# Performance work log

Hardware: AMD Instinct MI355X
Metric: run time of the kernel (lower is better)

Reference implementation:

```python
import math
import jax, jax.numpy as jnp
import numpy as np

SAMPLE_RATIO = 0.25
K_NN = 5


def grid_index(loc_orig, H, W):
    # loc in [-1,1] -> nearest grid cell index (row-major)
    loc = jnp.clip(loc_orig, -1.0, 1.0) * 0.5 + 0.5
    ix = jnp.clip(jnp.round(loc[..., 0] * (W - 1)).astype(jnp.int32), 0, W - 1)
    iy = jnp.clip(jnp.round(loc[..., 1] * (H - 1)).astype(jnp.int32), 0, H - 1)
    return iy * W + ix  # [B, N0]


def token2map(x, loc_orig, idx_agg, H, W):
    # scatter token features (replicated to original points) into HxW grid, cell-average
    B, N, C = x.shape
    N0 = idx_agg.shape[1]
    idx_hw = grid_index(loc_orig, H, W)
    off = jnp.arange(B, dtype=jnp.int32)[:, None]
    idx_hw_flat = (idx_hw + off * (H * W)).reshape(-1)
    value = jnp.ones((B * N0,), x.dtype)
    all_w = jax.ops.segment_sum(value, idx_hw_flat, num_segments=B * H * W) + 1e-6
    value = value / all_w[idx_hw_flat]
    x_src = jnp.take_along_axis(x, idx_agg[..., None], axis=1).reshape(B * N0, C)
    x_map = jax.ops.segment_sum(x_src * value[:, None], idx_hw_flat, num_segments=B * H * W)
    return x_map.reshape(B, H, W, C).transpose(0, 3, 1, 2)  # [B,C,H,W]


def map2token(x_map, N, loc_orig, idx_agg, agg_weight):
    # gather grid features back to tokens, weighted by per-token-normalized agg_weight
    B, C, H, W = x_map.shape
    N0 = idx_agg.shape[1]
    idx_hw = grid_index(loc_orig, H, W)
    off = jnp.arange(B, dtype=jnp.int32)[:, None]
    idx_tok_flat = (idx_agg + off * N).reshape(-1)
    idx_hw_flat = (idx_hw + off * (H * W)).reshape(-1)
    value = agg_weight.reshape(-1).astype(x_map.dtype)
    all_w = jax.ops.segment_sum(value, idx_tok_flat, num_segments=B * N) + 1e-6
    value = value / all_w[idx_tok_flat]
    feat = x_map.transpose(0, 2, 3, 1).reshape(B * H * W, C)[idx_hw_flat]
    out = jax.ops.segment_sum(feat * value[:, None], idx_tok_flat, num_segments=B * N)
    return out.reshape(B, N, C)


def cluster_dpc_knn(x, Ns, k):
    # DPC-KNN clustering (no_grad in original -> stop_gradient)
    B, N, C = x.shape
    x = jax.lax.stop_gradient(x)
    x2 = jnp.sum(x * x, axis=-1)
    d2 = x2[:, :, None] + x2[:, None, :] - 2.0 * jnp.einsum('bic,bjc->bij', x, x)
    dist = jnp.sqrt(jnp.maximum(d2, 0.0)) / jnp.sqrt(jnp.asarray(C, x.dtype))
    dist_nearest = -jax.lax.top_k(-dist, k)[0]                 # k smallest dists (incl self)
    density = jnp.exp(-jnp.mean(dist_nearest ** 2, axis=-1))    # [B,N]
    # deterministic tiny tie-break noise (original uses torch.rand*1e-6)
    density = density + jax.random.uniform(jax.random.key(42), density.shape, density.dtype) * 1e-6
    mask = (density[:, None, :] > density[:, :, None]).astype(x.dtype)
    dist_max = jnp.max(dist.reshape(B, -1), axis=-1)[:, None, None]
    dist_ind = jnp.min(dist * mask + dist_max * (1.0 - mask), axis=-1)
    score = dist_ind * density
    index_down = jax.lax.top_k(score, Ns)[1]                    # [B,Ns] cluster centers
    dist_c = jnp.take_along_axis(dist, index_down[:, :, None], axis=1)  # [B,Ns,N]
    idx_cluster = jnp.argmin(dist_c, axis=1).astype(jnp.int32)  # [B,N]
    # centers belong to their own cluster
    flat = (index_down + jnp.arange(B)[:, None] * N).reshape(-1)
    own = jnp.tile(jnp.arange(Ns, dtype=jnp.int32), B)
    idx_cluster = idx_cluster.reshape(-1).at[flat].set(own).reshape(B, N)
    return idx_cluster


def merge_tokens(x, idx_cluster, Ns, weight, idx_agg):
    # weighted average of tokens per cluster; propagate mapping/weights to original points
    B, N, C = x.shape
    idx = (idx_cluster + jnp.arange(B, dtype=jnp.int32)[:, None] * Ns).reshape(-1)
    w = weight.reshape(-1)
    all_w = jax.ops.segment_sum(w, idx, num_segments=B * Ns) + 1e-6
    nw = w / all_w[idx]
    x_merged = jax.ops.segment_sum(x.reshape(B * N, C) * nw[:, None], idx,
                                   num_segments=B * Ns).reshape(B, Ns, C)
    norm_weight = nw.reshape(B, N, 1)
    idx_agg_new = jnp.take_along_axis(idx_cluster, idx_agg, axis=1)          # [B,N0]
    weight_t = jnp.take_along_axis(norm_weight, idx_agg[..., None], axis=1)  # [B,N0,1]
    return x_merged, idx_agg_new, weight_t


def ctm_forward(x, loc_orig, idx_agg, agg_weight, conv_w, conv_b, skip_w, ln_g, ln_b,
                conf_w, conf_b, H, W):
    B, N, C = x.shape
    x_map = token2map(x, loc_orig, idx_agg, H, W)
    x_map = jax.lax.conv_general_dilated(
        x_map, conv_w, window_strides=(2, 2), padding=((1, 1), (1, 1)),
        dimension_numbers=('NCHW', 'OIHW', 'NCHW')) + conv_b[None, :, None, None]
    xt = map2token(x_map, N, loc_orig, idx_agg, agg_weight) + x @ skip_w.T
    mu = jnp.mean(xt, axis=-1, keepdims=True)
    var = jnp.mean((xt - mu) ** 2, axis=-1, keepdims=True)
    xt = (xt - mu) / jnp.sqrt(var + 1e-5) * ln_g + ln_b
    conf = xt @ conf_w.T + conf_b          # [B,N,1]
    weight = jnp.exp(conf)
    Ns = max(math.ceil(N * SAMPLE_RATIO), 1)
    idx_cluster = cluster_dpc_knn(xt, Ns, K_NN)
    x_down, idx_agg_down, weight_t = merge_tokens(xt, idx_cluster, Ns, weight, idx_agg)
    agg_weight_down = agg_weight * weight_t
    agg_weight_down = agg_weight_down / jnp.max(agg_weight_down, axis=1, keepdims=True)
    # down_block is identity in this reference
    return x_down, idx_agg_down, agg_weight_down


def setup_inputs() -> dict:
    key = jax.random.key(0)
    ks = jax.random.split(key, 10)
    B, N, C, C2, H, W = 4, 3136, 64, 128, 56, 56
    return {
        'x': jax.random.normal(ks[0], (B, N, C), jnp.float32),
        'loc_orig': jax.random.normal(ks[1], (B, N, 2), jnp.float32),
        'idx_agg': jax.random.randint(ks[2], (B, N), 0, N),
        'agg_weight': jax.random.uniform(ks[3], (B, N, 1), jnp.float32, 0.1, 1.0),
        'conv_w': jax.random.normal(ks[4], (C2, C, 3, 3), jnp.float32) * 0.02,
        'conv_b': jnp.zeros((C2,), jnp.float32),
        'skip_w': jax.random.normal(ks[5], (C2, C), jnp.float32) * 0.02,
        'ln_g': jnp.ones((C2,), jnp.float32),
        'ln_b': jnp.zeros((C2,), jnp.float32),
        'conf_w': jax.random.normal(ks[6], (1, C2), jnp.float32) * 0.02,
        'conf_b': jnp.zeros((1,), jnp.float32),
        'H': 56,
        'W': 56,
    }


def reference(x, loc_orig, idx_agg, agg_weight, conv_w, conv_b, skip_w, ln_g, ln_b,
              conf_w, conf_b, H, W):
    return ctm_forward(x, loc_orig, idx_agg, agg_weight, conv_w, conv_b, skip_w,
                       ln_g, ln_b, conf_w, conf_b, H, W)
```

## Files before the change

kernel.cpp:

```cpp
#include <hip/hip_runtime.h>
#include <math.h>
#include <float.h>

#define Bq   4
#define Nq   3136
#define Cq   64
#define C2q  128
#define Hq   56
#define Wq   56
#define HWq  (Hq*Wq)
#define HOq  28
#define WOq  28
#define HWOq (HOq*WOq)
#define NSq  784
#define KNN  5
#define BNq  (Bq*Nq)

#define T64   64
#define KC    32
#define NIT64 (Nq/T64)
#define NPAIR (NIT64*(NIT64+1)/2)
#define NSPL  8
#define NSPA  2
#define LDP   34

__device__ __constant__ int c_spl[NSPL + 1]  = {0, 7, 13, 19, 25, 31, 37, 43, 49};
__device__ __constant__ int c_spla[NSPA + 1] = {0, 7, 13};

typedef unsigned int   u32;
typedef unsigned long long u64;
typedef __attribute__((ext_vector_type(4))) double d64x4;

static __device__ __forceinline__ void atomicMaxPosD(double* p, double v) {
    atomicMax((u64*)p, (u64)__double_as_longlong(v));
}
static __device__ __forceinline__ int clampTok(int t) {
    return min(max(t, 0), Nq - 1);
}

static __device__ __forceinline__ u64 encD(double d) {
    u64 u = (u64)__double_as_longlong(d);
    return (u >> 63) ? ~u : (u | 0x8000000000000000ULL);
}
static __device__ __forceinline__ double decD(u64 u) {
    u64 o = (u >> 63) ? (u ^ 0x8000000000000000ULL) : ~u;
    return __longlong_as_double((long long)o);
}
#define ENC_DBL_MAX 0xFFEFFFFFFFFFFFFFULL

static __device__ __forceinline__ void ins5(double* a, double v) {
    if (v < a[KNN - 1]) {
        a[KNN - 1] = v;
        #pragma unroll
        for (int m = KNN - 1; m > 0; m--)
            if (a[m] < a[m - 1]) { double t = a[m]; a[m] = a[m - 1]; a[m - 1] = t; }
    }
}
static __device__ __forceinline__ void cex(double& a, double& b) {
    double lo = fmin(a, b), hi = fmax(a, b); a = lo; b = hi;
}
static __device__ __forceinline__ void merge5(double* a, const double* p) {
    double t0 = fmin(a[0], p[4]);
    double t1 = fmin(a[1], p[3]);
    double t2 = fmin(a[2], p[2]);
    double t3 = fmin(a[3], p[1]);
    double t4 = fmin(a[4], p[0]);
    cex(t0, t1); cex(t1, t2); cex(t2, t3); cex(t3, t4);
    cex(t0, t1); cex(t1, t2); cex(t2, t3);
    cex(t0, t1); cex(t1, t2);
    cex(t0, t1);
    a[0] = t0; a[1] = t1; a[2] = t2; a[3] = t3; a[4] = t4;
}

static __device__ __forceinline__ int mfma_mode_probe(int l4, int l15) {
    d64x4 p;
    #pragma unroll
    for (int v = 0; v < 4; v++) p[v] = 0.0;
    double a1 = (l4 == 0) ? (double)(16 * l15) : 0.0;
    double b1 = (l4 == 0) ? 1.0 : 0.0;
    p = __builtin_amdgcn_mfma_f64_16x16x4f64(a1, b1, p, 0, 0, 0);
    double a2 = (l4 == 0) ? 1.0 : 0.0;
    double b2 = (l4 == 0) ? (double)l15 : 0.0;
    p = __builtin_amdgcn_mfma_f64_16x16x4f64(a2, b2, p, 0, 0, 0);
    bool ok0 = true, ok1 = true;
    #pragma unroll
    for (int v = 0; v < 4; v++) {
        ok0 = ok0 && (p[v] == (double)(16 * (4 * l4 + v) + l15));
        ok1 = ok1 && (p[v] == (double)(16 * (l4 + 4 * v) + l15));
    }
    return __all(ok0) ? 0 : (__all(ok1) ? 1 : 2);
}

static __device__ __forceinline__ u32 rotl32(u32 x, int d) { return (x << d) | (x >> (32 - d)); }
static __device__ __forceinline__ float tf_uniform(int t) {
    const u32 k0 = 0u, k1 = 42u;
    const u32 ks2 = k0 ^ k1 ^ 0x1BD11BDAu;
    u32 ks[3] = { k0, k1, ks2 };
    bool lo = (t < 6272);
    u32 cx0 = lo ? (u32)t : (u32)(t - 6272);
    u32 cx1 = lo ? (u32)(t + 6272) : (u32)t;
    u32 x0 = cx0 + ks[0];
    u32 x1 = cx1 + ks[1];
    const int R0[4] = {13, 15, 26, 6};
    const int R1[4] = {17, 29, 16, 24};
// ... 125 lines not shown
    #pragma unroll 16
    for (int k = 0; k < Cq; k++) acc += (double)xr[k] * (double)sw[k];
    __shared__ double slot[4][2];
    double s = acc;
    #pragma unroll
    for (int m = 1; m <= 32; m <<= 1) s += __shfl_xor(s, m);
    if (lane == 0) slot[0][w] = s;
    __syncthreads();
    double mu = (slot[0][0] + slot[0][1]) * (1.0 / C2q);
    double d = acc - mu;
    s = d * d;
    #pragma unroll
    for (int m = 1; m <= 32; m <<= 1) s += __shfl_xor(s, m);
    if (lane == 0) slot[1][w] = s;
    __syncthreads();
    double var = (slot[1][0] + slot[1][1]) * (1.0 / C2q);
    double v = d / sqrt(var + 1e-5) * (double)lng[c] + (double)lnb[c];
    row[c] = v;
    s = v * v;
    #pragma unroll
    for (int m = 1; m <= 32; m <<= 1) s += __shfl_xor(s, m);
    if (lane == 0) slot[2][w] = s;
    double s2 = v * (double)confw[c];
    #pragma unroll
    for (int m = 1; m <= 32; m <<= 1) s2 += __shfl_xor(s2, m);
    if (lane == 0) slot[3][w] = s2;
    __syncthreads();
    if (c == 0) {
        x2o[bn] = slot[2][0] + slot[2][1];
        weightv[bn] = exp(slot[3][0] + slot[3][1] + (double)confb[0]);
    }
}


__global__ __launch_bounds__(256, 2)
void ctm_pass1(const double* __restrict__ xt, const double* __restrict__ x2,
               double* pbest, double* pmax) {
    __shared__ double sBB[2][T64][LDP];
    __shared__ double sx2j[2][T64];
    int blk = blockIdx.x;
    int b  = blk & (Bq - 1);
    int s  = (blk >> 2) & (NSPL - 1);
    int it = blk >> 5;
    int tid = threadIdx.x;
    const double* xtb = xt + (size_t)b * Nq * C2q;
    const double* x2b = x2 + (size_t)b * Nq;
    int i0 = it * T64;
    int jt_beg = c_spl[s], jt_end = c_spl[s + 1];

    int wv = tid >> 6, ln = tid & 63;
    int l15 = ln & 15, l4 = ln >> 4;
    int mode = mfma_mode_probe(l4, l15);

    if (mode < 2) {
        int rw[4];
        #pragma unroll
        for (int v = 0; v < 4; v++) rw[v] = (mode == 0) ? (4 * l4 + v) : (l4 + 4 * v);
        int rbase = i0 + wv * 16;
        double a_reg[4][8];
        const double* arow = xtb + (size_t)(i0 + wv * 16 + l15) * C2q + l4;
        #pragma unroll
        for (int kc = 0; kc < 4; kc++)
            #pragma unroll
            for (int st = 0; st < 8; st++)
                a_reg[kc][st] = arow[kc * KC + 4 * st];
        double x2i[4];
        #pragma unroll
        for (int v = 0; v < 4; v++) x2i[v] = x2b[rbase + rw[v]];
        double best[4][KNN]; double mx[4];
        #pragma unroll
        for (int v = 0; v < 4; v++) {
            mx[v] = -DBL_MAX;
            #pragma unroll
            for (int k = 0; k < KNN; k++) best[v][k] = DBL_MAX;
        }
        {
            int j0 = jt_beg * T64;
            #pragma unroll
            for (int w = 0; w < 4; w++) {
                int idx = tid + w * 256; int r = idx >> 4, c = (idx & 15) * 2;
                *(double2*)&sBB[0][r][c] = *(const double2*)&xtb[(size_t)(j0 + r) * C2q + c];
            }
            if (tid < T64) sx2j[0][tid] = x2b[j0 + tid];
        }
        __syncthreads();
        int q = 0;
        for (int jt = jt_beg; jt < jt_end; jt++) {
            int j0 = jt * T64;
            d64x4 acc[4];
            #pragma unroll
            for (int bc = 0; bc < 4; bc++)
                #pragma unroll
                for (int v = 0; v < 4; v++) acc[bc][v] = 0.0;
            #pragma unroll
            for (int kc = 0; kc < 4; kc++) {
                const int cb = kc & 1, nb = cb ^ 1, nkc = (kc + 1) & 3;
                const bool lastk = (kc == 3);
                bool hn = !lastk || (jt + 1 < jt_end);
                int nj0 = lastk ? j0 + T64 : j0;
                double2 sreg[4]; double xr = 0.0;
                if (hn) {
                    #pragma unroll
                    for (int w = 0; w < 4; w++) {
                        int idx = tid + w * 256; int r = idx >> 4, c = (idx & 15) * 2;
                        sreg[w] = *(const double2*)&xtb[(size_t)(nj0 + r) * C2q + nkc * KC + c];
                    }
                    if (lastk && tid < T64) xr = x2b[nj0 + tid];
                }
                #pragma unroll
                for (int st = 0; st < 8; st++) {
                    double av = a_reg[kc][st];
                    #pragma unroll
                    for (int bc = 0; bc < 4; bc++) {
                        double bv = sBB[cb][bc * 16 + l15][4 * st + l4];
                        acc[bc] = __builtin_amdgcn_mfma_f64_16x16x4f64(av, bv, acc[bc], 0, 0, 0);
                    }
                }
                if (hn) {
                    #pragma unroll
                    for (int w = 0; w < 4; w++) {
                        int idx = tid + w * 256; int r = idx >> 4, c = (idx & 15) * 2;
                        *(double2*)&sBB[nb][r][c] = sreg[w];
                    }
                    if (lastk && tid < T64) sx2j[q ^ 1][tid] = xr;
                }
                __syncthreads();
            }
            #pragma unroll
            for (int bc = 0; bc < 4; bc++) {
                double xj = sx2j[q][bc * 16 + l15];
                #pragma unroll
                for (int v = 0; v < 4; v++) {
                    double d2 = x2i[v] + xj - 2.0 * acc[bc][v];
                    mx[v] = fmax(mx[v], d2);
                    ins5(best[v], d2);
                }
            }
            q ^= 1;
        }
        for (int m = 1; m <= 8; m <<= 1) {
            #pragma unroll
            for (int v = 0; v < 4; v++) {
                double p[KNN];
                #pragma unroll
                for (int k = 0; k < KNN; k++) p[k] = __shfl_xor(best[v][k], m);
                mx[v] = fmax(mx[v], __shfl_xor(mx[v], m));
                merge5(best[v], p);
            }
        }
        if (l15 == 0) {
            #pragma unroll
            for (int v = 0; v < 4; v++) {
                int gi = b * Nq + rbase + rw[v];
                size_t base = ((size_t)s * BNq + gi) * KNN;
                #pragma unroll
                for (int k = 0; k < KNN; k++) pbest[base + k] = best[v][k];
                pmax[(size_t)s * BNq + gi] = mx[v];
            }
        }
    } else {
        double (*sA)[LDP] = sBB[0];
        double (*sB)[LDP] = sBB[1];
        int tx = tid & 15, ty = tid >> 4;
        double x2i[4];
        #pragma unroll
        for (int r = 0; r < 4; r++) x2i[r] = x2b[i0 + ty + 16 * r];
        double best[4][KNN]; double mx[4];
        #pragma unroll
        for (int r = 0; r < 4; r++) {
            mx[r] = -DBL_MAX;
            #pragma unroll
            for (int k = 0; k < KNN; k++) best[r][k] = DBL_MAX;
        }
        for (int jt = jt_beg; jt < jt_end; jt++) {
            int j0 = jt * T64;
            double acc[4][4];
            #pragma unroll
            for (int r = 0; r < 4; r++)
                #pragma unroll
                for (int q = 0; q < 4; q++) acc[r][q] = 0.0;
            for (int kc = 0; kc < 4; kc++) {
                __syncthreads();
                #pragma unroll
                for (int idx = tid; idx < T64 * KC / 2; idx += 256) {
                    int r = idx >> 4, c = (idx & 15) * 2;
                    *(double2*)&sA[r][c] = *(const double2*)&xtb[(size_t)(i0 + r) * C2q + kc * KC + c];
                    *(double2*)&sB[r][c] = *(const double2*)&xtb[(size_t)(j0 + r) * C2q + kc * KC + c];
                }
                if (kc == 0 && tid < T64) sx2j[0][tid] = x2b[j0 + tid];
                __syncthreads();
                #pragma unroll 4
                for (int cc = 0; cc < KC; cc += 2) {
                    double2 xi[4], xj[4];
                    #pragma unroll
                    for (int r = 0; r < 4; r++) xi[r] = *(const double2*)&sA[ty + 16 * r][cc];
                    #pragma unroll
                    for (int q = 0; q < 4; q++) xj[q] = *(const double2*)&sB[tx + 16 * q][cc];
                    #pragma unroll
                    for (int r = 0; r < 4; r++)
                        #pragma unroll
                        for (int q = 0; q < 4; q++) acc[r][q] += xi[r].x * xj[q].x;
                    #pragma unroll
                    for (int r = 0; r < 4; r++)
                        #pragma unroll
                        for (int q = 0; q < 4; q++) acc[r][q] += xi[r].y * xj[q].y;
                }
            }
            #pragma unroll
            for (int r = 0; r < 4; r++)
                #pragma unroll
                for (int q = 0; q < 4; q++) {
                    double d2 = x2i[r] + sx2j[0][tx + 16 * q] - 2.0 * acc[r][q];
                    mx[r] = fmax(mx[r], d2);
                    ins5(best[r], d2);
                }
        }
        for (int m = 1; m <= 8; m <<= 1) {
            #pragma unroll
            for (int r = 0; r < 4; r++) {
                double p[KNN];
                #pragma unroll
                for (int k = 0; k < KNN; k++) p[k] = __shfl_xor(best[r][k], m);
                mx[r] = fmax(mx[r], __shfl_xor(mx[r], m));
                merge5(best[r], p);
            }
        }
        if (tx == 0) {
            #pragma unroll
            for (int r = 0; r < 4; r++) {
                int gi = b * Nq + i0 + ty + 16 * r;
                size_t base = ((size_t)s * BNq + gi) * KNN;
                #pragma unroll
                for (int k = 0; k < KNN; k++) pbest[base + k] = best[r][k];
                pmax[(size_t)s * BNq + gi] = mx[r];
            }
        }
    }
}

__global__ void ctm_merge1(const double* __restrict__ pbest, const double* __restrict__ pmax,
                           double* density, double* maxd2) {
    int t = blockIdx.x * blockDim.x + threadIdx.x;
    if (t >= BNq) return;
    double a[KNN];
    #pragma unroll
    for (int k = 0; k < KNN; k++) a[k] = pbest[(size_t)t * KNN + k];
    double mxv = pmax[t];
    #pragma unroll
    for (int s = 1; s < NSPL; s++) {
        double p[KNN];
        #pragma unroll
        for (int k = 0; k < KNN; k++) p[k] = pbest[((size_t)s * BNq + t) * KNN + k];
        merge5(a, p);
        mxv = fmax(mxv, pmax[(size_t)s * BNq + t]);
    }
    double sum = 0.0;
    #pragma unroll
    for (int k = 0; k < KNN; k++) sum += fmax(a[k], 0.0);
    density[t] = exp(-sum / (double)(C2q * KNN)) + (double)(tf_uniform(t) * 1e-6f);
    atomicMaxPosD(&maxd2[t / Nq], mxv);
}

__global__ __launch_bounds__(1024)
void ctm_sortd(const double* __restrict__ density, int* perm) {
    __shared__ double s[4096];
    __shared__ int   si[4096];
    int b = blockIdx.x, tid = threadIdx.x;
    for (int i = tid; i < 4096; i += 1024) {
        if (i < Nq) {
            double v = density[b * Nq + i];
            s[i] = isnan(v) ? -DBL_MAX : v;
            si[i] = i;
        } else { s[i] = -DBL_MAX; si[i] = 0x7fffffff; }
    }
    __syncthreads();
    for (int k = 2; k <= 4096; k <<= 1) {
        for (int j = k >> 1; j > 0; j >>= 1) {
            for (int i = tid; i < 4096; i += 1024) {
                int ixj = i ^ j;
                if (ixj > i) {
                    double s1 = s[i], s2 = s[ixj];
                    int i1 = si[i], i2 = si[ixj];
                    bool before_ij = (s1 > s2) || (s1 == s2 && i1 < i2);
                    bool before_ji = (s2 > s1) || (s2 == s1 && i2 < i1);
                    bool doswap = ((i & k) == 0) ? before_ji : before_ij;
                    if (doswap) { s[i] = s2; s[ixj] = s1; si[i] = i2; si[ixj] = i1; }
                }
            }
            __syncthreads();
        }
    }
    for (int t = tid; t < Nq; t += 1024) {
        int v = si[t];
        perm[b * Nq + t] = ((unsigned)v < (unsigned)Nq) ? v : 0;
    }
}

__global__ void ctm_initmin(u64* pmin2u) {
    int t = blockIdx.x * blockDim.x + threadIdx.x;
    if (t < BNq) pmin2u[t] = ENC_DBL_MAX;
}

__global__ __launch_bounds__(256, 2)
void ctm_pass2t(const double* __restrict__ xt, const double* __restrict__ x2,
                const double* __restrict__ density, const int* __restrict__ perm,
                u64* pmin2u) {
    __shared__ double sBB[2][T64][LDP];
    __shared__ double sx2j[T64];
    __shared__ double sdj[T64];
    __shared__ int    sI[T64];
    __shared__ int    sJ[T64];
    __shared__ double sp[4][T64];
    int blk = blockIdx.x;
    int b = blk & (Bq - 1);
    int p = blk >> 2;
    int it = (int)((sqrt(8.0 * (double)p + 1.0) - 1.0) * 0.5);
    while ((it + 1) * (it + 2) / 2 <= p) ++it;
    while (it * (it + 1) / 2 > p) --it;
    int jt = p - it * (it + 1) / 2;
    int i0 = it * T64, j0 = jt * T64;
    int tid = threadIdx.x;
    const double* xtb = xt + (size_t)b * Nq * C2q;
    const double* x2b = x2 + (size_t)b * Nq;
    const double* db  = density + (size_t)b * Nq;
    const int* pb = perm + b * Nq;
    if (tid < T64) sI[tid] = pb[i0 + tid];
    else if (tid < 2 * T64) sJ[tid - T64] = pb[j0 + tid - T64];
    __syncthreads();
    int wv = tid >> 6, ln = tid & 63;
    int l15 = ln & 15, l4 = ln >> 4;
    int mode = mfma_mode_probe(l4, l15);

    if (mode < 2) {
        int rw[4];
        #pragma unroll
        for (int v = 0; v < 4; v++) rw[v] = (mode == 0) ? (4 * l4 + v) : (l4 + 4 * v);
        int rloc = wv * 16;
        double a_reg[4][8];
        const double* arow = xtb + (size_t)sI[rloc + l15] * C2q + l4;
        #pragma unroll
        for (int kc = 0; kc < 4; kc++)
            #pragma unroll
            for (int st = 0; st < 8; st++)
                a_reg[kc][st] = arow[kc * KC + 4 * st];
        double x2i[4], di[4];
        #pragma unroll
        for (int v = 0; v < 4; v++) {
            int o = sI[rloc + rw[v]];
            x2i[v] = x2b[o];
            di[v]  = db[o];
        }
        #pragma unroll
        for (int w = 0; w < 4; w++) {
            int idx = tid + w * 256; int r = idx >> 4, c = (idx & 15) * 2;
            *(double2*)&sBB[0][r][c] = *(const double2*)&xtb[(size_t)sJ[r] * C2q + c];
        }
        if (tid < T64) { int o = sJ[tid]; sx2j[tid] = x2b[o]; sdj[tid] = db[o]; }
        __syncthreads();
        d64x4 acc[4];
        #pragma unroll
        for (int bc = 0; bc < 4; bc++)
            #pragma unroll
            for (int v = 0; v < 4; v++) acc[bc][v] = 0.0;
        #pragma unroll
        for (int kc = 0; kc < 4; kc++) {
            const int cb = kc & 1, nb = cb ^ 1;
            const bool hn = (kc < 3);
            double2 sreg[4];
            if (hn) {
                #pragma unroll
                for (int w = 0; w < 4; w++) {
                    int idx = tid + w * 256; int r = idx >> 4, c = (idx & 15) * 2;
                    sreg[w] = *(const double2*)&xtb[(size_t)sJ[r] * C2q + (kc + 1) * KC + c];
                }
            }
            #pragma unroll
            for (int st = 0; st < 8; st++) {
                double av = a_reg[kc][st];
                #pragma unroll
                for (int bc = 0; bc < 4; bc++) {
                    double bv = sBB[cb][bc * 16 + l15][4 * st + l4];
                    acc[bc] = __builtin_amdgcn_mfma_f64_16x16x4f64(av, bv, acc[bc], 0, 0, 0);
                }
            }
            if (hn) {
                #pragma unroll
                for (int w = 0; w < 4; w++) {
                    int idx = tid + w * 256; int r = idx >> 4, c = (idx & 15) * 2;
                    *(double2*)&sBB[nb][r][c] = sreg[w];
                }
            }
            __syncthreads();
        }
        double mn[4];
        #pragma unroll
        for (int v = 0; v < 4; v++) mn[v] = DBL_MAX;
        #pragma unroll
        for (int bc = 0; bc < 4; bc++) {
            double xj = sx2j[bc * 16 + l15];
            double dj = sdj[bc * 16 + l15];
            #pragma unroll
            for (int v = 0; v < 4; v++) {
                double d2 = x2i[v] + xj - 2.0 * acc[bc][v];
                if (dj > di[v]) mn[v] = fmin(mn[v], d2);
            }
        }
        for (int m = 1; m <= 8; m <<= 1) {
            #pragma unroll
            for (int v = 0; v < 4; v++) mn[v] = fmin(mn[v], __shfl_xor(mn[v], m));
        }
        if (l15 == 0) {
            #pragma unroll
            for (int v = 0; v < 4; v++)
                if (mn[v] < DBL_MAX)
                    atomicMin(&pmin2u[b * Nq + i0 + rloc + rw[v]], encD(mn[v]));
        }
    } else {
        int rl = tid & 63;
        int cg = tid >> 6;
        int ro = sI[rl];
        double x2i = x2b[ro];
        double di = db[ro];
        const double* xr = xtb + (size_t)ro * C2q;
        double mn = DBL_MAX;
        for (int cc = 0; cc < 16; cc++) {
            int co = sJ[cg * 16 + cc];
            if (db[co] > di) {
                const double* xc = xtb + (size_t)co * C2q;
                double dot = 0.0;
                for (int k = 0; k < C2q; k++) dot += xr[k] * xc[k];
                mn = fmin(mn, x2i + x2b[co] - 2.0 * dot);
            }
        }
        sp[cg][rl] = mn;
        __syncthreads();
        if (cg == 0) {
            mn = fmin(fmin(sp[0][rl], sp[1][rl]), fmin(sp[2][rl], sp[3][rl]));
            if (mn < DBL_MAX)
                atomicMin(&pmin2u[b * Nq + i0 + rl], encD(mn));
        }
    }
}

__global__ void ctm_merge2t(const u64* __restrict__ pmin2u, const double* __restrict__ maxd2,
                            const double* __restrict__ density, const int* __restrict__ perm,
                            double* score) {
    int t = blockIdx.x * blockDim.x + threadIdx.x;
    if (t >= BNq) return;
    int b = t / Nq;
    double m = decD(pmin2u[t]);
    double mm = fmin(maxd2[b], m);
    int orig = b * Nq + perm[t];
    score[orig] = sqrt(fmax(mm, 0.0)) / sqrt((double)C2q) * density[orig];
}

__global__ __launch_bounds__(1024)
void ctm_sort(const double* __restrict__ score, int* index_down) {
    __shared__ double s[4096];
    __shared__ int   si[4096];
    int b = blockIdx.x, tid = threadIdx.x;
    for (int i = tid; i < 4096; i += 1024) {
        if (i < Nq) {
            double v = score[b * Nq + i];
            s[i] = isnan(v) ? -DBL_MAX : v;
// ... 168 lines not shown
            }
            #pragma unroll
            for (int r = 0; r < 4; r++)
                #pragma unroll
                for (int q = 0; q < 4; q++) {
                    int sc = j0 + tx + 16 * q;
                    double d = fmax(x2i[r] + sx2c[tx + 16 * q] - 2.0 * acc[r][q], 0.0);
                    if (sc < NSq && (d < bd[r] || (d == bd[r] && sc < bs[r]))) { bd[r] = d; bs[r] = sc; }
                }
        }
        for (int m = 1; m <= 8; m <<= 1) {
            #pragma unroll
            for (int r = 0; r < 4; r++) {
                double pd = __shfl_xor(bd[r], m);
                int    ps = __shfl_xor(bs[r], m);
                if (pd < bd[r] || (pd == bd[r] && ps < bs[r])) { bd[r] = pd; bs[r] = ps; }
            }
        }
        if (tx == 0) {
            #pragma unroll
            for (int r = 0; r < 4; r++) {
                int gi = b * Nq + i0 + ty + 16 * r;
                pbd[(size_t)s * BNq + gi] = bd[r];
                pbs[(size_t)s * BNq + gi] = bs[r];
            }
        }
    }
}

__global__ void ctm_merge3(const double* __restrict__ pbd, const int* __restrict__ pbs,
                           int* idx_cluster) {
    int t = blockIdx.x * blockDim.x + threadIdx.x;
    if (t >= BNq) return;
    double d0 = pbd[t];          int s0 = pbs[t];
    double d1 = pbd[BNq + t];    int s1 = pbs[BNq + t];
    bool take1 = (d1 < d0) || (d1 == d0 && s1 < s0);
    idx_cluster[t] = take1 ? s1 : s0;
}

__global__ void ctm_override(const int* __restrict__ index_down, int* idx_cluster) {
    int t = blockIdx.x * blockDim.x + threadIdx.x;
    if (t >= Bq * NSq) return;
    int b = t / NSq, sc = t - b * NSq;
    int j = index_down[t];
    if ((unsigned)j < (unsigned)Nq) idx_cluster[b * Nq + j] = sc;
}

__global__ void ctm_zeromerged(double* xmerged) {
    int t = blockIdx.x * blockDim.x + threadIdx.x;
    if (t < Bq * NSq * C2q) xmerged[t] = 0.0;
}

__global__ void ctm_merge_w(const int* __restrict__ idx_cluster, const double* __restrict__ weightv,
                            double* allwc) {
    int t = blockIdx.x * blockDim.x + threadIdx.x;
    if (t >= BNq) return;
    int b = t / Nq;
    int sc = min(max(idx_cluster[t], 0), NSq - 1);
    atomicAdd(&allwc[b * NSq + sc], weightv[t]);
}

__global__ void ctm_merge_x(const int* __restrict__ idx_cluster, const double* __restrict__ weightv,
                            const double* __restrict__ allwc, const double* __restrict__ xt,
                            double* nw, double* xmerged) {
    int id = blockIdx.x * blockDim.x + threadIdx.x;
    if (id >= BNq * C2q) return;
    int t = id / C2q, c = id - t * C2q;
    int b = t / Nq;
    int sc = min(max(idx_cluster[t], 0), NSq - 1);
    double nv = weightv[t] / (allwc[b * NSq + sc] + 1e-6);
// ... 45 lines not shown
    (void)in_sizes; (void)n_in;

    char* w = (char*)d_ws;
    size_t off = 0;
    auto alloc = [&](size_t bytes) -> void* {
        void* p = w + off; off = (off + bytes + 255) & ~(size_t)255; return p;
    };

    int*    cnt56   = (int*)   alloc((size_t)BNq * 4);
    double* allwtok = (double*)alloc((size_t)BNq * 8);
    double* xt      = (double*)alloc((size_t)BNq * C2q * 8);
    double* arena   = (double*)alloc((size_t)Bq * HWq * Cq * 8);
    double* allwc   = (double*)alloc((size_t)Bq * NSq * 8);
    double* maxawd  = (double*)alloc((size_t)Bq * 8);
    double* maxd2   = (double*)alloc((size_t)Bq * 8);
    size_t zero_bytes = off;
    int*    cell56   = (int*)   alloc((size_t)BNq * 4);
    int*    cell28   = (int*)   alloc((size_t)BNq * 4);
    double* xmap28T  = (double*)alloc((size_t)Bq * HWOq * C2q * 8);
    float*  wT       = (float*) alloc((size_t)C2q * Cq * 9 * 4);
    double* x2       = (double*)alloc((size_t)BNq * 8);
    double* density  = (double*)alloc((size_t)BNq * 8);
    double* score    = (double*)alloc((size_t)BNq * 8);
    int*    indexdn  = (int*)   alloc((size_t)Bq * NSq * 4);
    int*    idxclu   = (int*)   alloc((size_t)BNq * 4);
    double* nw       = (double*)alloc((size_t)BNq * 8);
    double* weightv  = (double*)alloc((size_t)BNq * 8);
    double* awd      = (double*)alloc((size_t)BNq * 8);
    double* pbest    = (double*)alloc((size_t)NSPL * BNq * KNN * 8);
    double* pmax     = (double*)alloc((size_t)NSPL * BNq * 8);
    double* pbd      = (double*)alloc((size_t)NSPA * BNq * 8);
    int*    pbs      = (int*)   alloc((size_t)NSPA * BNq * 4);
    size_t required = off;

    int* perm   = (int*)pbest;
    u64* pmin2u = (u64*)((char*)pbest + 131072);

    const int tb = 256;
    float* out = (float*)d_out;

    if (ws_size < required) {
        ctm_fallback<<<(out_size + tb - 1) / tb, tb, 0, stream>>>(out, out_size);
        return;
    }

    double* xmap56T = arena;
    double* xmerged = arena;

    hipMemsetAsync(d_ws, 0, zero_bytes, stream);

    ctm_prep<<<(BNq + tb - 1) / tb, tb, 0, stream>>>(loc, idxag, aggw, cell56, cell28, cnt56, allwtok);
    ctm_wt<<<((C2q * Cq * 9) + tb - 1) / tb, tb, 0, stream>>>(convw, wT);
    ctm_t2m<<<((BNq * Cq) + tb - 1) / tb, tb, 0, stream>>>(x, idxag, cell56, cnt56, xmap56T);
    ctm_conv<<<Bq * (HWOq / 2), 256, 0, stream>>>(xmap56T, wT, convb, xmap28T);
    ctm_m2t<<<((BNq * C2q) + tb - 1) / tb, tb, 0, stream>>>(xmap28T, aggw, idxag, cell28, allwtok, xt);
    ctm_finalize<<<BNq, C2q, 0, stream>>>(xt, x, skipw, lng, lnb, confw, confb, x2, weightv);
    ctm_pass1<<<Bq * NSPL * NIT64, 256, 0, stream>>>(xt, x2, pbest, pmax);
    ctm_merge1<<<(BNq + tb - 1) / tb, tb, 0, stream>>>(pbest, pmax, density, maxd2);
    ctm_sortd<<<Bq, 1024, 0, stream>>>(density, perm);
    ctm_initmin<<<(BNq + tb - 1) / tb, tb, 0, stream>>>(pmin2u);
    ctm_pass2t<<<Bq * NPAIR, 256, 0, stream>>>(xt, x2, density, perm, pmin2u);
    ctm_merge2t<<<(BNq + tb - 1) / tb, tb, 0, stream>>>(pmin2u, maxd2, density, perm, score);
    ctm_sort<<<Bq, 1024, 0, stream>>>(score, indexdn);
    ctm_assign<<<Bq * NSPA * NIT64, 256, 0, stream>>>(xt, x2, indexdn, pbd, pbs);
    ctm_merge3<<<(BNq + tb - 1) / tb, tb, 0, stream>>>(pbd, pbs, idxclu);
    ctm_override<<<((Bq * NSq) + tb - 1) / tb, tb, 0, stream>>>(indexdn, idxclu);
    ctm_zeromerged<<<((Bq * NSq * C2q) + tb - 1) / tb, tb, 0, stream>>>(xmerged);
    ctm_merge_w<<<(BNq + tb - 1) / tb, tb, 0, stream>>>(idxclu, weightv, allwc);
    ctm_merge_x<<<((BNq * C2q) + tb - 1) / tb, tb, 0, stream>>>(idxclu, weightv, allwc, xt, nw, xmerged);

    ctm_out0<<<((Bq * NSq * C2q) + tb - 1) / tb, tb, 0, stream>>>(xmerged, out);
    ctm_out12<<<(BNq + tb - 1) / tb, tb, 0, stream>>>(idxag, idxclu, nw, aggw,
                                                      out + (size_t)Bq * NSq * C2q, awd, maxawd);
    ctm_out2<<<(BNq + tb - 1) / tb, tb, 0, stream>>>(awd, maxawd,
                                                     out + (size_t)Bq * NSq * C2q + BNq);
}
```

Baseline: 1.218 ms.

## Exploit distance symmetry in kNN pass with triangular tiles and atomic top-5 merge

```diff
diff --git a/kernel.cpp b/kernel.cpp
--- a/kernel.cpp
+++ b/kernel.cpp
@@ -24,7 +24,6 @@
 #define NSPA  2
 #define LDP   34
 
-__device__ __constant__ int c_spl[NSPL + 1]  = {0, 7, 13, 19, 25, 31, 37, 43, 49};
 __device__ __constant__ int c_spla[NSPA + 1] = {0, 7, 13};
 
 typedef unsigned int   u32;
@@ -70,6 +69,28 @@
     cex(t0, t1); cex(t1, t2);
     cex(t0, t1);
     a[0] = t0; a[1] = t1; a[2] = t2; a[3] = t3; a[4] = t4;
+}
+
+static __device__ __forceinline__ void cas5_insert1(u64* s, double v) {
+    u64 e = encD(v);
+    if (e >= ((volatile u64*)s)[4]) return;
+    #pragma unroll
+    for (int j = 0; j < KNN; j++) {
+        u64 old = atomicMin(&s[j], e);
+        if (old > e) e = old;
+    }
+}
+static __device__ __forceinline__ void cas5_insertList(u64* s, const double* lst) {
+    u64 s4 = ((volatile u64*)s)[4];
+    for (int k = 0; k < KNN; k++) {
+        u64 e = encD(lst[k]);
+        if (e >= s4) break;
+        #pragma unroll
+        for (int j = 0; j < KNN; j++) {
+            u64 old = atomicMin(&s[j], e);
+            if (old > e) e = old;
+        }
+    }
 }
 
 static __device__ __forceinline__ int mfma_mode_probe(int l4, int l15) {
@@ -261,22 +282,30 @@
     }
 }
 
+__global__ void ctm_inits(u64* best5, u64* pmin2u) {
+    int t = blockIdx.x * blockDim.x + threadIdx.x;
+    if (t < BNq * KNN) best5[t] = ENC_DBL_MAX;
+    if (t < BNq) pmin2u[t] = ENC_DBL_MAX;
+}
 
 __global__ __launch_bounds__(256, 2)
-void ctm_pass1(const double* __restrict__ xt, const double* __restrict__ x2,
-               double* pbest, double* pmax) {
+void ctm_pass1t(const double* __restrict__ xt, const double* __restrict__ x2,
+                u64* best5, double* maxd2) {
     __shared__ double sBB[2][T64][LDP];
-    __shared__ double sx2j[2][T64];
+    __shared__ double sx2j[T64];
+    __shared__ double swmax[4];
     int blk = blockIdx.x;
-    int b  = blk & (Bq - 1);
-    int s  = (blk >> 2) & (NSPL - 1);
-    int it = blk >> 5;
+    int b = blk & (Bq - 1);
+    int p = blk >> 2;
+    int it = (int)((sqrt(8.0 * (double)p + 1.0) - 1.0) * 0.5);
+    while ((it + 1) * (it + 2) / 2 <= p) ++it;
+    while (it * (it + 1) / 2 > p) --it;
+    int jt = p - it * (it + 1) / 2;
+    const bool diag = (jt == it);
+    int i0 = it * T64, j0 = jt * T64;
     int tid = threadIdx.x;
     const double* xtb = xt + (size_t)b * Nq * C2q;
     const double* x2b = x2 + (size_t)b * Nq;
-    int i0 = it * T64;
-    int jt_beg = c_spl[s], jt_end = c_spl[s + 1];
-
     int wv = tid >> 6, ln = tid & 63;
     int l15 = ln & 15, l4 = ln >> 4;
     int mode = mfma_mode_probe(l4, l15);
@@ -287,7 +316,7 @@
         for (int v = 0; v < 4; v++) rw[v] = (mode == 0) ? (4 * l4 + v) : (l4 + 4 * v);
         int rbase = i0 + wv * 16;
         double a_reg[4][8];
-        const double* arow = xtb + (size_t)(i0 + wv * 16 + l15) * C2q + l4;
+        const double* arow = xtb + (size_t)(rbase + l15) * C2q + l4;
         #pragma unroll
         for (int kc = 0; kc < 4; kc++)
             #pragma unroll
@@ -296,198 +325,130 @@
         double x2i[4];
         #pragma unroll
         for (int v = 0; v < 4; v++) x2i[v] = x2b[rbase + rw[v]];
-        double best[4][KNN]; double mx[4];
+        #pragma unroll
+        for (int w = 0; w < 4; w++) {
+            int idx = tid + w * 256; int r = idx >> 4, c = (idx & 15) * 2;
+            *(double2*)&sBB[0][r][c] = *(const double2*)&xtb[(size_t)(j0 + r) * C2q + c];
+        }
+        if (tid < T64) sx2j[tid] = x2b[j0 + tid];
+        __syncthreads();
+        d64x4 acc[4];
+        #pragma unroll
+        for (int bc = 0; bc < 4; bc++)
+            #pragma unroll
+            for (int v = 0; v < 4; v++) acc[bc][v] = 0.0;
+        #pragma unroll
+        for (int kc = 0; kc < 4; kc++) {
+            const int cb = kc & 1, nb = cb ^ 1;
+            const bool hn = (kc < 3);
+            double2 sreg[4];
+            if (hn) {
+                #pragma unroll
+                for (int w = 0; w < 4; w++) {
+                    int idx = tid + w * 256; int r = idx >> 4, c = (idx & 15) * 2;
+                    sreg[w] = *(const double2*)&xtb[(size_t)(j0 + r) * C2q + (kc + 1) * KC + c];
+                }
+            }
+            #pragma unroll
+            for (int st = 0; st < 8; st++) {
+                double av = a_reg[kc][st];
+                #pragma unroll
+                for (int bc = 0; bc < 4; bc++) {
+                    double bv = sBB[cb][bc * 16 + l15][4 * st + l4];
+                    acc[bc] = __builtin_amdgcn_mfma_f64_16x16x4f64(av, bv, acc[bc], 0, 0, 0);
+                }
+            }
+            if (hn) {
+                #pragma unroll
+                for (int w = 0; w < 4; w++) {
+                    int idx = tid + w * 256; int r = idx >> 4, c = (idx & 15) * 2;
+                    *(double2*)&sBB[nb][r][c] = sreg[w];
+                }
+            }
+            __syncthreads();
+        }
+        double d2v[4][4];
+        #pragma unroll
+        for (int bc = 0; bc < 4; bc++) {
+            double xj = sx2j[bc * 16 + l15];
+            #pragma unroll
+            for (int v = 0; v < 4; v++)
+                d2v[bc][v] = x2i[v] + xj - 2.0 * acc[bc][v];
+        }
+        double mx = -DBL_MAX;
+        #pragma unroll
+        for (int bc = 0; bc < 4; bc++)
+            #pragma unroll
+            for (int v = 0; v < 4; v++) mx = fmax(mx, d2v[bc][v]);
+        #pragma unroll
+        for (int m = 1; m <= 32; m <<= 1) mx = fmax(mx, __shfl_xor(mx, m));
+        if (ln == 0) swmax[wv] = mx;
         #pragma unroll
         for (int v = 0; v < 4; v++) {
-            mx[v] = -DBL_MAX;
-            #pragma unroll
-            for (int k = 0; k < KNN; k++) best[v][k] = DBL_MAX;
-        }
-        {
-            int j0 = jt_beg * T64;
-            #pragma unroll
-            for (int w = 0; w < 4; w++) {
-                int idx = tid + w * 256; int r = idx >> 4, c = (idx & 15) * 2;
-                *(double2*)&sBB[0][r][c] = *(const double2*)&xtb[(size_t)(j0 + r) * C2q + c];
-            }
-            if (tid < T64) sx2j[0][tid] = x2b[j0 + tid];
+            double lst[KNN];
+            #pragma unroll
+            for (int k = 0; k < KNN; k++) lst[k] = DBL_MAX;
+            #pragma unroll
+            for (int bc = 0; bc < 4; bc++) ins5(lst, d2v[bc][v]);
+            for (int m = 1; m <= 8; m <<= 1) {
+                double pl[KNN];
+                #pragma unroll
+                for (int k = 0; k < KNN; k++) pl[k] = __shfl_xor(lst[k], m);
+                merge5(lst, pl);
+            }
+            if (l15 == 0)
+                cas5_insertList(&best5[((size_t)(b * Nq + rbase + rw[v])) * KNN], lst);
+        }
+        if (!diag) {
+            #pragma unroll
+            for (int bc = 0; bc < 4; bc++) {
+                double lst[KNN];
+                #pragma unroll
+                for (int k = 0; k < KNN; k++) lst[k] = DBL_MAX;
+                #pragma unroll
+                for (int v = 0; v < 4; v++) ins5(lst, d2v[bc][v]);
+                for (int m = 16; m <= 32; m <<= 1) {
+                    double pl[KNN];
+                    #pragma unroll
+                    for (int k = 0; k < KNN; k++) pl[k] = __shfl_xor(lst[k], m);
+                    merge5(lst, pl);
+                }
+                if (l4 == 0)
+                    cas5_insertList(&best5[((size_t)(b * Nq + j0 + bc * 16 + l15)) * KNN], lst);
+            }
         }
         __syncthreads();
-        int q = 0;
-        for (int jt = jt_beg; jt < jt_end; jt++) {
-            int j0 = jt * T64;
-            d64x4 acc[4];
-            #pragma unroll
-            for (int bc = 0; bc < 4; bc++)
-                #pragma unroll
-                for (int v = 0; v < 4; v++) acc[bc][v] = 0.0;
-            #pragma unroll
-            for (int kc = 0; kc < 4; kc++) {
-                const int cb = kc & 1, nb = cb ^ 1, nkc = (kc + 1) & 3;
-                const bool lastk = (kc == 3);
-                bool hn = !lastk || (jt + 1 < jt_end);
-                int nj0 = lastk ? j0 + T64 : j0;
-                double2 sreg[4]; double xr = 0.0;
-                if (hn) {
-                    #pragma unroll
-                    for (int w = 0; w < 4; w++) {
-                        int idx = tid + w * 256; int r = idx >> 4, c = (idx & 15) * 2;
-                        sreg[w] = *(const double2*)&xtb[(size_t)(nj0 + r) * C2q + nkc * KC + c];
-                    }
-                    if (lastk && tid < T64) xr = x2b[nj0 + tid];
-                }
-                #pragma unroll
-                for (int st = 0; st < 8; st++) {
-                    double av = a_reg[kc][st];
-                    #pragma unroll
-                    for (int bc = 0; bc < 4; bc++) {
-                        double bv = sBB[cb][bc * 16 + l15][4 * st + l4];
-                        acc[bc] = __builtin_amdgcn_mfma_f64_16x16x4f64(av, bv, acc[bc], 0, 0, 0);
-                    }
-                }
-                if (hn) {
-                    #pragma unroll
-                    for (int w = 0; w < 4; w++) {
-                        int idx = tid + w * 256; int r = idx >> 4, c = (idx & 15) * 2;
-                        *(double2*)&sBB[nb][r][c] = sreg[w];
-                    }
-                    if (lastk && tid < T64) sx2j[q ^ 1][tid] = xr;
-                }
-                __syncthreads();
-            }
-            #pragma unroll
-            for (int bc = 0; bc < 4; bc++) {
-                double xj = sx2j[q][bc * 16 + l15];
-                #pragma unroll
-                for (int v = 0; v < 4; v++) {
-                    double d2 = x2i[v] + xj - 2.0 * acc[bc][v];
-                    mx[v] = fmax(mx[v], d2);
-                    ins5(best[v], d2);
-                }
-            }
-            q ^= 1;
-        }
-        for (int m = 1; m <= 8; m <<= 1) {
-            #pragma unroll
-            for (int v = 0; v < 4; v++) {
-                double p[KNN];
-                #pragma unroll
-                for (int k = 0; k < KNN; k++) p[k] = __shfl_xor(best[v][k], m);
-                mx[v] = fmax(mx[v], __shfl_xor(mx[v], m));
-                merge5(best[v], p);
-            }
-        }
-        if (l15 == 0) {
-            #pragma unroll
-            for (int v = 0; v < 4; v++) {
-                int gi = b * Nq + rbase + rw[v];
-                size_t base = ((size_t)s * BNq + gi) * KNN;
-                #pragma unroll
-                for (int k = 0; k < KNN; k++) pbest[base + k] = best[v][k];
-                pmax[(size_t)s * BNq + gi] = mx[v];
-            }
+        if (tid == 0) {
+            double m = fmax(fmax(swmax[0], swmax[1]), fmax(swmax[2], swmax[3]));
+            atomicMaxPosD(&maxd2[b], fmax(m, 0.0));
         }
     } else {
-        double (*sA)[LDP] = sBB[0];
-        double (*sB)[LDP] = sBB[1];
-        int tx = tid & 15, ty = tid >> 4;
-        double x2i[4];
-        #pragma unroll
-        for (int r = 0; r < 4; r++) x2i[r] = x2b[i0 + ty + 16 * r];
-        double best[4][KNN]; double mx[4];
-        #pragma unroll
-        for (int r = 0; r < 4; r++) {
-            mx[r] = -DBL_MAX;
-            #pragma unroll
-            for (int k = 0; k < KNN; k++) best[r][k] = DBL_MAX;
-        }
-        for (int jt = jt_beg; jt < jt_end; jt++) {
-            int j0 = jt * T64;
-            double acc[4][4];
-            #pragma unroll
-            for (int r = 0; r < 4; r++)
-                #pragma unroll
-                for (int q = 0; q < 4; q++) acc[r][q] = 0.0;
-            for (int kc = 0; kc < 4; kc++) {
-                __syncthreads();
-                #pragma unroll
-                for (int idx = tid; idx < T64 * KC / 2; idx += 256) {
-                    int r = idx >> 4, c = (idx & 15) * 2;
-                    *(double2*)&sA[r][c] = *(const double2*)&xtb[(size_t)(i0 + r) * C2q + kc * KC + c];
-                    *(double2*)&sB[r][c] = *(const double2*)&xtb[(size_t)(j0 + r) * C2q + kc * KC + c];
-                }
-                if (kc == 0 && tid < T64) sx2j[0][tid] = x2b[j0 + tid];
-                __syncthreads();
-                #pragma unroll 4
-                for (int cc = 0; cc < KC; cc += 2) {
-                    double2 xi[4], xj[4];
-                    #pragma unroll
-                    for (int r = 0; r < 4; r++) xi[r] = *(const double2*)&sA[ty + 16 * r][cc];
-                    #pragma unroll
-                    for (int q = 0; q < 4; q++) xj[q] = *(const double2*)&sB[tx + 16 * q][cc];
-                    #pragma unroll
-                    for (int r = 0; r < 4; r++)
-                        #pragma unroll
-                        for (int q = 0; q < 4; q++) acc[r][q] += xi[r].x * xj[q].x;
-                    #pragma unroll
-                    for (int r = 0; r < 4; r++)
-                        #pragma unroll
-                        for (int q = 0; q < 4; q++) acc[r][q] += xi[r].y * xj[q].y;
-                }
-            }
-            #pragma unroll
-            for (int r = 0; r < 4; r++)
-                #pragma unroll
-                for (int q = 0; q < 4; q++) {
-                    double d2 = x2i[r] + sx2j[0][tx + 16 * q] - 2.0 * acc[r][q];
-                    mx[r] = fmax(mx[r], d2);
-                    ins5(best[r], d2);
-                }
-        }
-        for (int m = 1; m <= 8; m <<= 1) {
-            #pragma unroll
-            for (int r = 0; r < 4; r++) {
-                double p[KNN];
-                #pragma unroll
-                for (int k = 0; k < KNN; k++) p[k] = __shfl_xor(best[r][k], m);
-                mx[r] = fmax(mx[r], __shfl_xor(mx[r], m));
-                merge5(best[r], p);
-            }
-        }
-        if (tx == 0) {
-            #pragma unroll
-            for (int r = 0; r < 4; r++) {
-                int gi = b * Nq + i0 + ty + 16 * r;
-                size_t base = ((size_t)s * BNq + gi) * KNN;
-                #pragma unroll
-                for (int k = 0; k < KNN; k++) pbest[base + k] = best[r][k];
-                pmax[(size_t)s * BNq + gi] = mx[r];
-            }
-        }
-    }
-}
-
-__global__ void ctm_merge1(const double* __restrict__ pbest, const double* __restrict__ pmax,
-                           double* density, double* maxd2) {
+        int rl = tid & 63, cq = tid >> 6;
+        int gi = i0 + rl;
+        double x2i = x2b[gi];
+        const double* xr = xtb + (size_t)gi * C2q;
+        double mx = -DBL_MAX;
+        for (int cc = 0; cc < 16; cc++) {
+            int gj = j0 + cq * 16 + cc;
+            const double* xc = xtb + (size_t)gj * C2q;
+            double dot = 0.0;
+            for (int k = 0; k < C2q; k++) dot += xr[k] * xc[k];
+            double d2 = x2i + x2b[gj] - 2.0 * dot;
+            mx = fmax(mx, d2);
+            cas5_insert1(&best5[(size_t)(b * Nq + gi) * KNN], d2);
+            if (!diag) cas5_insert1(&best5[(size_t)(b * Nq + gj) * KNN], d2);
+        }
+        atomicMaxPosD(&maxd2[b], fmax(mx, 0.0));
+    }
+}
+
+__global__ void ctm_density(const u64* __restrict__ best5, double* density) {
     int t = blockIdx.x * blockDim.x + threadIdx.x;
     if (t >= BNq) return;
-    double a[KNN];
-    #pragma unroll
-    for (int k = 0; k < KNN; k++) a[k] = pbest[(size_t)t * KNN + k];
-    double mxv = pmax[t];
-    #pragma unroll
-    for (int s = 1; s < NSPL; s++) {
-        double p[KNN];
-        #pragma unroll
-        for (int k = 0; k < KNN; k++) p[k] = pbest[((size_t)s * BNq + t) * KNN + k];
-        merge5(a, p);
-        mxv = fmax(mxv, pmax[(size_t)s * BNq + t]);
-    }
     double sum = 0.0;
     #pragma unroll
-    for (int k = 0; k < KNN; k++) sum += fmax(a[k], 0.0);
+    for (int k = 0; k < KNN; k++) sum += fmax(decD(best5[(size_t)t * KNN + k]), 0.0);
     density[t] = exp(-sum / (double)(C2q * KNN)) + (double)(tf_uniform(t) * 1e-6f);
-    atomicMaxPosD(&maxd2[t / Nq], mxv);
 }
 
 __global__ __launch_bounds__(1024)
@@ -523,11 +484,6 @@
         int v = si[t];
         perm[b * Nq + t] = ((unsigned)v < (unsigned)Nq) ? v : 0;
     }
-}
-
-__global__ void ctm_initmin(u64* pmin2u) {
-    int t = blockIdx.x * blockDim.x + threadIdx.x;
-    if (t < BNq) pmin2u[t] = ENC_DBL_MAX;
 }
 
 __global__ __launch_bounds__(256, 2)
@@ -1008,9 +964,11 @@
     double* pbd      = (double*)alloc((size_t)NSPA * BNq * 8);
     int*    pbs      = (int*)   alloc((size_t)NSPA * BNq * 4);
     size_t required = off;
-
-    int* perm   = (int*)pbest;
-    u64* pmin2u = (u64*)((char*)pbest + 131072);
+    (void)pmax;
+
+    u64* best5  = (u64*)pbest;
+    u64* pmin2u = (u64*)((char*)pbest + 524288);
+    int* perm   = (int*)((char*)pbest + 655360);
 
     const int tb = 256;
     float* out = (float*)d_out;
@@ -1031,10 +989,10 @@
     ctm_conv<<<Bq * (HWOq / 2), 256, 0, stream>>>(xmap56T, wT, convb, xmap28T);
     ctm_m2t<<<((BNq * C2q) + tb - 1) / tb, tb, 0, stream>>>(xmap28T, aggw, idxag, cell28, allwtok, xt);
     ctm_finalize<<<BNq, C2q, 0, stream>>>(xt, x, skipw, lng, lnb, confw, confb, x2, weightv);
-    ctm_pass1<<<Bq * NSPL * NIT64, 256, 0, stream>>>(xt, x2, pbest, pmax);
-    ctm_merge1<<<(BNq + tb - 1) / tb, tb, 0, stream>>>(pbest, pmax, density, maxd2);
+    ctm_inits<<<((BNq * KNN) + tb - 1) / tb, tb, 0, stream>>>(best5, pmin2u);
+    ctm_pass1t<<<Bq * NPAIR, 256, 0, stream>>>(xt, x2, best5, maxd2);
+    ctm_density<<<(BNq + tb - 1) / tb, tb, 0, stream>>>(best5, density);
     ctm_sortd<<<Bq, 1024, 0, stream>>>(density, perm);
-    ctm_initmin<<<(BNq + tb - 1) / tb, tb, 0, stream>>>(pmin2u);
     ctm_pass2t<<<Bq * NPAIR, 256, 0, stream>>>(xt, x2, density, perm, pmin2u);
     ctm_merge2t<<<(BNq + tb - 1) / tb, tb, 0, stream>>>(pmin2u, maxd2, density, perm, score);
     ctm_sort<<<Bq, 1024, 0, stream>>>(score, indexdn);
```

New measurement: 1.318 ms. 8.2% more time.

## Process four column tiles per block in pass2t to reuse row fragments

Applied to the files above, without the earlier changes.

```diff
diff --git a/kernel.cpp b/kernel.cpp
--- a/kernel.cpp
+++ b/kernel.cpp
@@ -19,13 +19,18 @@
 #define T64   64
 #define KC    32
 #define NIT64 (Nq/T64)
-#define NPAIR (NIT64*(NIT64+1)/2)
 #define NSPL  8
 #define NSPA  2
 #define LDP   34
+#define CH2   4
+#define NCH2  325
 
 __device__ __constant__ int c_spl[NSPL + 1]  = {0, 7, 13, 19, 25, 31, 37, 43, 49};
 __device__ __constant__ int c_spla[NSPA + 1] = {0, 7, 13};
+__device__ __constant__ int c_p2start[NIT64 + 1] = {
+    0,1,2,3,4,6,8,10,12,15,18,21,24,28,32,36,40,45,50,55,
+    60,66,72,78,84,91,98,105,112,120,128,136,144,153,162,171,180,190,200,210,
+    220,231,242,253,264,276,288,300,312,325};
 
 typedef unsigned int   u32;
 typedef unsigned long long u64;
@@ -535,26 +540,32 @@
                 const double* __restrict__ density, const int* __restrict__ perm,
                 u64* pmin2u) {
     __shared__ double sBB[2][T64][LDP];
-    __shared__ double sx2j[T64];
-    __shared__ double sdj[T64];
+    __shared__ double sx2j[CH2][T64];
+    __shared__ double sdj[CH2][T64];
     __shared__ int    sI[T64];
-    __shared__ int    sJ[T64];
-    __shared__ double sp[4][T64];
+    __shared__ int    sJall[CH2][T64];
     int blk = blockIdx.x;
     int b = blk & (Bq - 1);
-    int p = blk >> 2;
-    int it = (int)((sqrt(8.0 * (double)p + 1.0) - 1.0) * 0.5);
-    while ((it + 1) * (it + 2) / 2 <= p) ++it;
-    while (it * (it + 1) / 2 > p) --it;
-    int jt = p - it * (it + 1) / 2;
-    int i0 = it * T64, j0 = jt * T64;
+    int q = blk >> 2;
+    int it = 0;
+    while (c_p2start[it + 1] <= q) ++it;
+    int jt_beg = (q - c_p2start[it]) * CH2;
+    int jt_end = min(jt_beg + CH2, it + 1);
+    int nt = jt_end - jt_beg;
+    int i0 = it * T64;
     int tid = threadIdx.x;
     const double* xtb = xt + (size_t)b * Nq * C2q;
     const double* x2b = x2 + (size_t)b * Nq;
     const double* db  = density + (size_t)b * Nq;
     const int* pb = perm + b * Nq;
     if (tid < T64) sI[tid] = pb[i0 + tid];
-    else if (tid < 2 * T64) sJ[tid - T64] = pb[j0 + tid - T64];
+    for (int idx = tid; idx < nt * T64; idx += 256) {
+        int t = idx >> 6, r = idx & 63;
+        int o = pb[(jt_beg + t) * T64 + r];
+        sJall[t][r] = o;
+        sx2j[t][r] = x2b[o];
+        sdj[t][r]  = db[o];
+    }
     __syncthreads();
     int wv = tid >> 6, ln = tid & 63;
     int l15 = ln & 15, l4 = ln >> 4;
@@ -572,66 +583,68 @@
             #pragma unroll
             for (int st = 0; st < 8; st++)
                 a_reg[kc][st] = arow[kc * KC + 4 * st];
-        double x2i[4], di[4];
+        double x2i[4], di[4], mn[4];
         #pragma unroll
         for (int v = 0; v < 4; v++) {
             int o = sI[rloc + rw[v]];
             x2i[v] = x2b[o];
             di[v]  = db[o];
+            mn[v]  = DBL_MAX;
         }
         #pragma unroll
         for (int w = 0; w < 4; w++) {
             int idx = tid + w * 256; int r = idx >> 4, c = (idx & 15) * 2;
-            *(double2*)&sBB[0][r][c] = *(const double2*)&xtb[(size_t)sJ[r] * C2q + c];
-        }
-        if (tid < T64) { int o = sJ[tid]; sx2j[tid] = x2b[o]; sdj[tid] = db[o]; }
+            *(double2*)&sBB[0][r][c] = *(const double2*)&xtb[(size_t)sJall[0][r] * C2q + c];
+        }
         __syncthreads();
-        d64x4 acc[4];
-        #pragma unroll
-        for (int bc = 0; bc < 4; bc++)
-            #pragma unroll
-            for (int v = 0; v < 4; v++) acc[bc][v] = 0.0;
-        #pragma unroll
-        for (int kc = 0; kc < 4; kc++) {
-            const int cb = kc & 1, nb = cb ^ 1;
-            const bool hn = (kc < 3);
-            double2 sreg[4];
-            if (hn) {
-                #pragma unroll
-                for (int w = 0; w < 4; w++) {
-                    int idx = tid + w * 256; int r = idx >> 4, c = (idx & 15) * 2;
-                    sreg[w] = *(const double2*)&xtb[(size_t)sJ[r] * C2q + (kc + 1) * KC + c];
-                }
-            }
-            #pragma unroll
-            for (int st = 0; st < 8; st++) {
-                double av = a_reg[kc][st];
-                #pragma unroll
-                for (int bc = 0; bc < 4; bc++) {
-                    double bv = sBB[cb][bc * 16 + l15][4 * st + l4];
-                    acc[bc] = __builtin_amdgcn_mfma_f64_16x16x4f64(av, bv, acc[bc], 0, 0, 0);
-                }
-            }
-            if (hn) {
-                #pragma unroll
-                for (int w = 0; w < 4; w++) {
-                    int idx = tid + w * 256; int r = idx >> 4, c = (idx & 15) * 2;
-                    *(double2*)&sBB[nb][r][c] = sreg[w];
-                }
-            }
-            __syncthreads();
-        }
-        double mn[4];
-        #pragma unroll
-        for (int v = 0; v < 4; v++) mn[v] = DBL_MAX;
-        #pragma unroll
-        for (int bc = 0; bc < 4; bc++) {
-            double xj = sx2j[bc * 16 + l15];
-            double dj = sdj[bc * 16 + l15];
-            #pragma unroll
-            for (int v = 0; v < 4; v++) {
-                double d2 = x2i[v] + xj - 2.0 * acc[bc][v];
-                if (dj > di[v]) mn[v] = fmin(mn[v], d2);
+        for (int tl = 0; tl < nt; tl++) {
+            d64x4 acc[4];
+            #pragma unroll
+            for (int bc = 0; bc < 4; bc++)
+                #pragma unroll
+                for (int v = 0; v < 4; v++) acc[bc][v] = 0.0;
+            #pragma unroll
+            for (int kc = 0; kc < 4; kc++) {
+                const int cb = kc & 1, nb = cb ^ 1, nkc = (kc + 1) & 3;
+                const bool lastk = (kc == 3);
+                int ntl = lastk ? tl + 1 : tl;
+                bool hn = !lastk || (tl + 1 < nt);
+                int stl = hn ? ntl : tl;
+                double2 sreg[4];
+                if (hn) {
+                    #pragma unroll
+                    for (int w = 0; w < 4; w++) {
+                        int idx = tid + w * 256; int r = idx >> 4, c = (idx & 15) * 2;
+                        sreg[w] = *(const double2*)&xtb[(size_t)sJall[stl][r] * C2q + nkc * KC + c];
+                    }
+                }
+                #pragma unroll
+                for (int st = 0; st < 8; st++) {
+                    double av = a_reg[kc][st];
+                    #pragma unroll
+                    for (int bc = 0; bc < 4; bc++) {
+                        double bv = sBB[cb][bc * 16 + l15][4 * st + l4];
+                        acc[bc] = __builtin_amdgcn_mfma_f64_16x16x4f64(av, bv, acc[bc], 0, 0, 0);
+                    }
+                }
+                if (hn) {
+                    #pragma unroll
+                    for (int w = 0; w < 4; w++) {
+                        int idx = tid + w * 256; int r = idx >> 4, c = (idx & 15) * 2;
+                        *(double2*)&sBB[nb][r][c] = sreg[w];
+                    }
+                }
+                __syncthreads();
+            }
+            #pragma unroll
+            for (int bc = 0; bc < 4; bc++) {
+                double xj = sx2j[tl][bc * 16 + l15];
+                double dj = sdj[tl][bc * 16 + l15];
+                #pragma unroll
+                for (int v = 0; v < 4; v++) {
+                    double d2 = x2i[v] + xj - 2.0 * acc[bc][v];
+                    if (dj > di[v]) mn[v] = fmin(mn[v], d2);
+                }
             }
         }
         for (int m = 1; m <= 8; m <<= 1) {
@@ -645,6 +658,7 @@
                     atomicMin(&pmin2u[b * Nq + i0 + rloc + rw[v]], encD(mn[v]));
         }
     } else {
+        double (*sp)[T64] = (double(*)[T64])&sBB[0][0][0];
         int rl = tid & 63;
         int cg = tid >> 6;
         int ro = sI[rl];
@@ -652,13 +666,15 @@
         double di = db[ro];
         const double* xr = xtb + (size_t)ro * C2q;
         double mn = DBL_MAX;
-        for (int cc = 0; cc < 16; cc++) {
-            int co = sJ[cg * 16 + cc];
-            if (db[co] > di) {
-                const double* xc = xtb + (size_t)co * C2q;
-                double dot = 0.0;
-                for (int k = 0; k < C2q; k++) dot += xr[k] * xc[k];
-                mn = fmin(mn, x2i + x2b[co] - 2.0 * dot);
+        for (int tl = 0; tl < nt; tl++) {
+            for (int cc = 0; cc < 16; cc++) {
+                int co = sJall[tl][cg * 16 + cc];
+                if (db[co] > di) {
+                    const double* xc = xtb + (size_t)co * C2q;
+                    double dot = 0.0;
+                    for (int k = 0; k < C2q; k++) dot += xr[k] * xc[k];
+                    mn = fmin(mn, x2i + x2b[co] - 2.0 * dot);
+                }
             }
         }
         sp[cg][rl] = mn;
@@ -893,10 +909,14 @@
                            int* idx_cluster) {
     int t = blockIdx.x * blockDim.x + threadIdx.x;
     if (t >= BNq) return;
-    double d0 = pbd[t];          int s0 = pbs[t];
-    double d1 = pbd[BNq + t];    int s1 = pbs[BNq + t];
-    bool take1 = (d1 < d0) || (d1 == d0 && s1 < s0);
-    idx_cluster[t] = take1 ? s1 : s0;
+    double bd = pbd[t];          int bs = pbs[t];
+    #pragma unroll
+    for (int s = 1; s < NSPA; s++) {
+        double d = pbd[(size_t)s * BNq + t];
+        int    i = pbs[(size_t)s * BNq + t];
+        if (d < bd || (d == bd && i < bs)) { bd = d; bs = i; }
+    }
+    idx_cluster[t] = bs;
 }
 
 __global__ void ctm_override(const int* __restrict__ index_down, int* idx_cluster) {
@@ -1035,7 +1055,7 @@
     ctm_merge1<<<(BNq + tb - 1) / tb, tb, 0, stream>>>(pbest, pmax, density, maxd2);
     ctm_sortd<<<Bq, 1024, 0, stream>>>(density, perm);
     ctm_initmin<<<(BNq + tb - 1) / tb, tb, 0, stream>>>(pmin2u);
-    ctm_pass2t<<<Bq * NPAIR, 256, 0, stream>>>(xt, x2, density, perm, pmin2u);
+    ctm_pass2t<<<Bq * NCH2, 256, 0, stream>>>(xt, x2, density, perm, pmin2u);
     ctm_merge2t<<<(BNq + tb - 1) / tb, tb, 0, stream>>>(pmin2u, maxd2, density, perm, score);
     ctm_sort<<<Bq, 1024, 0, stream>>>(score, indexdn);
     ctm_assign<<<Bq * NSPA * NIT64, 256, 0, stream>>>(xt, x2, indexdn, pbd, pbs);
```

New measurement: 1.231 ms. Within noise of the previous version (+1.1%).
